# Kernel tuning notes

Measured on AMD Instinct MI355X. Metric: run time of the kernel, lower is better.

## Reference

```python
import jax, jax.numpy as jnp
import numpy as np

B, N, FIN, H, D = 2, 512, 128, 4, 64
NEG_SLOPE = 0.2


def setup_inputs() -> dict:
    key = jax.random.key(0)
    ks = jax.random.split(key, 5)
    x = jax.random.normal(ks[0], (B, N, FIN), dtype=jnp.float32)
    # xavier-ish scaled params
    W_proj = jax.random.normal(ks[1], (H, FIN, D), dtype=jnp.float32) * (1.0 / np.sqrt(FIN + D))
    b_proj = jnp.zeros((H, D), dtype=jnp.float32)
    W_cat_weight = jax.random.normal(ks[2], (H, D, 2 * D), dtype=jnp.float32) * (1.0 / np.sqrt(3 * D))
    W_cat_bias = jnp.zeros((H, D), dtype=jnp.float32)
    a = jax.random.normal(ks[3], (H, D), dtype=jnp.float32) * (1.0 / np.sqrt(D))
    bias_param = jnp.zeros((H * D,), dtype=jnp.float32)
    return {"x": x, "W_proj": W_proj, "b_proj": b_proj,
            "W_cat_weight": W_cat_weight, "W_cat_bias": W_cat_bias,
            "a": a, "bias_param": bias_param}


def reference(x, W_proj, b_proj, W_cat_weight, W_cat_bias, a, bias_param):
    # h[b,h,n,d] = W^h x_n + b^h
    h = jnp.einsum('bni,hid->bhnd', x, W_proj) + b_proj[None, :, None, :]
    d = h.shape[-1]
    # W_cat [h_i || h_j] == W1 h_i + W2 h_j  (avoids O(N^2*2D) concat tensor)
    W1 = W_cat_weight[:, :, :d]   # (H, D, D) acts on source node i
    W2 = W_cat_weight[:, :, d:]   # (H, D, D) acts on target node j
    zi = jnp.einsum('bhnd,hed->bhne', h, W1)  # (B,H,N,D)
    zj = jnp.einsum('bhnd,hed->bhne', h, W2)  # (B,H,N,D)
    # z[b,h,i,j,e] = zi[b,h,i,e] + zj[b,h,j,e] + bias, then LeakyReLU
    z = zi[:, :, :, None, :] + zj[:, :, None, :, :] + W_cat_bias[None, :, None, None, :]
    z = jnp.where(z >= 0, z, NEG_SLOPE * z)
    # e[b,h,i,j] = a_h . z
    e = jnp.einsum('bhije,he->bhij', z, a)
    attn = jax.nn.softmax(e, axis=-1)          # softmax over neighbors j
    out = jnp.einsum('bhij,bhjd->bhid', attn, h)  # (B,H,N,D)
    b_, h_, n_, d_ = out.shape
    out = out.transpose(0, 2, 1, 3).reshape(b_, n_, h_ * d_)  # concat heads
    out = out + bias_param
    return out
```

## Files before the change

kernel.cpp:

```cpp
#include <hip/hip_runtime.h>
#include <hip/hip_bf16.h>

#define NN 512
#define FIN 128
#define HH 4
#define DD 64
#define SW 68


__global__ __launch_bounds__(256) void proj_kernel(
    const float* __restrict__ x, const float* __restrict__ Wp,
    const float* __restrict__ bp, const float* __restrict__ Wc,
    const float* __restrict__ Wcb, const float* __restrict__ a,
    float* __restrict__ h_ws, float* __restrict__ azi_ws, float* __restrict__ azj_ws,
    float* __restrict__ adi_ws, float* __restrict__ adj_ws)
{
    int blk = blockIdx.x;
    int bh = blk >> 6;
    int n0 = (blk & 63) << 3;
    int b = bh >> 2, hh = bh & 3;

    __shared__ float xs[8 * FIN];
    __shared__ float hs[8][DD];
    __shared__ float Wcs[DD][2 * DD + 1];

    int t = threadIdx.x;

    ((float4*)xs)[t] = ((const float4*)(x + ((size_t)b * NN + n0) * FIN))[t];
    {
        const float4* wg = (const float4*)(Wc + (size_t)hh * DD * 2 * DD);
        #pragma unroll
        for (int k = 0; k < 8; ++k) {
            int idx = t + 256 * k;
            int r = idx >> 5, c4 = (idx & 31) * 4;
            float4 v = wg[idx];
            Wcs[r][c4] = v.x; Wcs[r][c4 + 1] = v.y;
            Wcs[r][c4 + 2] = v.z; Wcs[r][c4 + 3] = v.w;
        }
    }
    __syncthreads();

    int e = t & 63, w = t >> 6;
    const float* Wph = Wp + (size_t)hh * FIN * DD;
    float bpv = bp[hh * DD + e];
    float acc0 = bpv, acc1 = bpv;
    #pragma unroll 8
    for (int i = 0; i < FIN; ++i) {
        float wv = Wph[i * DD + e];
        acc0 = fmaf(xs[w * FIN + i], wv, acc0);
        acc1 = fmaf(xs[(w + 4) * FIN + i], wv, acc1);
    }
    hs[w][e] = acc0; hs[w + 4][e] = acc1;
    float* hg = h_ws + ((size_t)bh * NN + n0) * DD;
    hg[w * DD + e] = acc0; hg[(w + 4) * DD + e] = acc1;
    __syncthreads();

    float zb = Wcb[hh * DD + e];
    float zi0 = zb, zi1 = zb, zj0 = 0.f, zj1 = 0.f;
    #pragma unroll 8
    for (int d2 = 0; d2 < DD; ++d2) {
        float w1 = Wcs[e][d2];
        float w2 = Wcs[e][DD + d2];
        float h0 = hs[w][d2], h1 = hs[w + 4][d2];
        zi0 = fmaf(h0, w1, zi0); zi1 = fmaf(h1, w1, zi1);
        zj0 = fmaf(h0, w2, zj0); zj1 = fmaf(h1, w2, zj1);
    }

    float av = a[hh * DD + e];
    float p0 = av * zi0, p1 = av * zi1, q0 = av * zj0, q1 = av * zj1;
    #pragma unroll
    for (int off = 32; off; off >>= 1) {
        p0 += __shfl_xor(p0, off); p1 += __shfl_xor(p1, off);
        q0 += __shfl_xor(q0, off); q1 += __shfl_xor(q1, off);
    }
    if (e == 0) {
        adi_ws[bh * NN + n0 + w]     = 0.6f * p0;
        adi_ws[bh * NN + n0 + w + 4] = 0.6f * p1;
        adj_ws[bh * NN + n0 + w]     = 0.6f * q0;
        adj_ws[bh * NN + n0 + w + 4] = 0.6f * q1;
    }

    unsigned long long mask = __ballot(av >= 0.f);
    int np = __popcll(mask);
    int GP = (np + 3) >> 2;
    int below = __popcll(mask & ((1ull << e) - 1ull));
    int slot = (av >= 0.f) ? below : (4 * GP + (e - below));
    float pav = __builtin_fabsf(av);

    float* azib = azi_ws + ((size_t)bh * NN + n0) * SW;
    float* azjb = azj_ws + ((size_t)bh * NN + n0) * SW;
    azib[w * SW + slot]       = pav * zi0;
    azib[(w + 4) * SW + slot] = pav * zi1;
    azjb[w * SW + slot]       = pav * zj0;
    azjb[(w + 4) * SW + slot] = pav * zj1;
    int p1c = 4 * GP - np;
    if (e < 4) {
        int psl = (e < p1c) ? (np + e) : (4 * GP + 64 - np + (e - p1c));
        azib[w * SW + psl] = 0.f; azib[(w + 4) * SW + psl] = 0.f;
        azjb[w * SW + psl] = 0.f; azjb[(w + 4) * SW + psl] = 0.f;
    }
}

#define AZJ 0
#define HT  2176
#define ADJ 4224
__global__ __launch_bounds__(256) void attn6(
    const float* __restrict__ h_ws, const float* __restrict__ azi_ws,
    const float* __restrict__ azj_ws, const float* __restrict__ adi_ws,
    const float* __restrict__ adj_ws, const float* __restrict__ a,
    float* __restrict__ pacc, float* __restrict__ pm, float* __restrict__ ps)
{
    int blk = blockIdx.x;
    int js = blk & 15, is_ = (blk >> 4) & 7, bh = blk >> 7;
    int i0 = is_ << 6, j0 = js << 5, hh = bh & 3;
    int t = threadIdx.x, lane = t & 63, w = t >> 6;

    __shared__ float smA[64 * 68];
    __shared__ float eP[32 * 68];

    {
        const float4* src = (const float4*)(azi_ws + ((size_t)bh * NN + i0) * SW);
        float4* dst = (float4*)smA;
        #pragma unroll
        for (int k = 0; k < 5; ++k) {
            int idx = t + 256 * k;
            if (idx < 1088) dst[idx] = src[idx];
        }
    }
    __syncthreads();
    float4 azi4[17];
    #pragma unroll
    for (int k = 0; k < 17; ++k)
        azi4[k] = *(const float4*)&smA[lane * SW + 4 * k];
    float adiv = adi_ws[bh * NN + i0 + lane];
    __syncthreads();

    {
        const float4* sj = (const float4*)(azj_ws + ((size_t)bh * NN + j0) * SW);
        #pragma unroll
        for (int k = 0; k < 3; ++k) {
            int idx = t + 256 * k;
            if (idx < 544) ((float4*)&smA[AZJ])[idx] = sj[idx];
        }
        const float4* sh = (const float4*)(h_ws + ((size_t)bh * NN + j0) * DD);
        ((float4*)&smA[HT])[t]       = sh[t];
        ((float4*)&smA[HT])[t + 256] = sh[t + 256];
        if (t < 32) smA[ADJ + t] = adj_ws[bh * NN + j0 + t];
    }

    float av_e = a[hh * DD + lane];
    unsigned long long mask = __ballot(av_e >= 0.f);
    int GP = (__popcll(mask) + 3) >> 2;

    __syncthreads();

    #pragma unroll
    for (int jj = 0; jj < 8; ++jj) {
        int j = 8 * w + jj;
        const float4* aj = (const float4*)&smA[AZJ + j * SW];
        float adjv = smA[ADJ + j];
        float c0 = 0.f, c1 = 0.f, c2 = 0.f, c3 = 0.f;
        #pragma unroll
        for (int k = 0; k < 17; ++k) {
            float4 A = aj[k];
            float sg = (k < GP) ? 0.4f : -0.4f;
            c0 = fmaf(sg, __builtin_fabsf(azi4[k].x + A.x), c0);
            c1 = fmaf(sg, __builtin_fabsf(azi4[k].y + A.y), c1);
            c2 = fmaf(sg, __builtin_fabsf(azi4[k].z + A.z), c2);
            c3 = fmaf(sg, __builtin_fabsf(azi4[k].w + A.w), c3);
        }
        eP[j * SW + lane] = adiv + adjv + ((c0 + c1) + (c2 + c3));
    }
    __syncthreads();

    {
        int il = lane & 15, jq = lane >> 4;
        int iL = 16 * w + il;
        float e8[8];
        float m = -1e30f;
        #pragma unroll
        for (int jj = 0; jj < 8; ++jj) {
            e8[jj] = eP[(jq * 8 + jj) * SW + iL];
            m = fmaxf(m, e8[jj]);
        }
        m = fmaxf(m, __shfl_xor(m, 16));
        m = fmaxf(m, __shfl_xor(m, 32));
        float s = 0.f;
        #pragma unroll
        for (int jj = 0; jj < 8; ++jj) {
            float p = __expf(e8[jj] - m);
            s += p;
            eP[(jq * 8 + jj) * SW + iL] = p;
        }
        s += __shfl_xor(s, 16);
        s += __shfl_xor(s, 32);
        if (jq == 0) {
            pm[js * 4096 + bh * NN + i0 + iL] = m;
            ps[js * 4096 + bh * NN + i0 + iL] = s;
        }
    }
    __syncthreads();

    float acc[16];
    #pragma unroll
    for (int ii = 0; ii < 16; ++ii) acc[ii] = 0.f;
    #pragma unroll 8
    for (int j = 0; j < 32; ++j) {
        float hv = smA[HT + j * 64 + lane];
        const float4* pp = (const float4*)&eP[j * SW + 16 * w];
        float4 p0 = pp[0], p1 = pp[1], p2 = pp[2], p3 = pp[3];
        acc[0]  = fmaf(p0.x, hv, acc[0]);  acc[1]  = fmaf(p0.y, hv, acc[1]);
        acc[2]  = fmaf(p0.z, hv, acc[2]);  acc[3]  = fmaf(p0.w, hv, acc[3]);
        acc[4]  = fmaf(p1.x, hv, acc[4]);  acc[5]  = fmaf(p1.y, hv, acc[5]);
        acc[6]  = fmaf(p1.z, hv, acc[6]);  acc[7]  = fmaf(p1.w, hv, acc[7]);
        acc[8]  = fmaf(p2.x, hv, acc[8]);  acc[9]  = fmaf(p2.y, hv, acc[9]);
        acc[10] = fmaf(p2.z, hv, acc[10]); acc[11] = fmaf(p2.w, hv, acc[11]);
        acc[12] = fmaf(p3.x, hv, acc[12]); acc[13] = fmaf(p3.y, hv, acc[13]);
        acc[14] = fmaf(p3.z, hv, acc[14]); acc[15] = fmaf(p3.w, hv, acc[15]);
    }

    float* pb = pacc + ((size_t)(js * 8 + bh) * NN + i0 + 16 * w) * DD + lane;
    #pragma unroll
    for (int ii = 0; ii < 16; ++ii)
        pb[(size_t)ii * DD] = acc[ii];
}

__global__ __launch_bounds__(256) void combine_kernel(
    const float* __restrict__ pacc, const float* __restrict__ pm,
    const float* __restrict__ ps, const float* __restrict__ bias_param,
    float* __restrict__ out)
{
    int tid = blockIdx.x * 256 + threadIdx.x;
    int d = tid & 63;
    int row = tid >> 6;
    int bh = row >> 9, n = row & 511;
    int b = bh >> 2, hh = bh & 3;
    float mv[16];
    float m = -1e30f;
    #pragma unroll
    for (int p = 0; p < 16; ++p) { mv[p] = pm[p * 4096 + row]; m = fmaxf(m, mv[p]); }
    float denom = 0.f, acc = 0.f;
    #pragma unroll
    for (int p = 0; p < 16; ++p) {
        float wgt = __expf(mv[p] - m);
        denom = fmaf(ps[p * 4096 + row], wgt, denom);
        acc = fmaf(pacc[(size_t)p * 262144 + (size_t)row * 64 + d], wgt, acc);
    }
    out[((size_t)b * NN + n) * (HH * DD) + hh * DD + d] =
        acc / denom + bias_param[hh * DD + d];
}

extern "C" void kernel_launch(void* const* d_in, const int* in_sizes, int n_in,
                              void* d_out, int out_size, void* d_ws, size_t ws_size,
                              hipStream_t stream) {
    const float* x    = (const float*)d_in[0];
    const float* Wp   = (const float*)d_in[1];
    const float* bp   = (const float*)d_in[2];
    const float* Wc   = (const float*)d_in[3];
    const float* Wcb  = (const float*)d_in[4];
    const float* a    = (const float*)d_in[5];
    const float* bpar = (const float*)d_in[6];
    float* out = (float*)d_out;

    float* ws     = (float*)d_ws;
    float* h_ws   = ws;
    float* azi_ws = ws + 262144;
    float* azj_ws = ws + 540672;
    float* adi_ws = ws + 819200;
    float* adj_ws = ws + 823296;
    float* pacc   = ws + 827392;
    float* pm     = ws + 5021696;
    float* ps     = ws + 5087232;

    proj_kernel<<<dim3(512), dim3(256), 0, stream>>>(
        x, Wp, bp, Wc, Wcb, a, h_ws, azi_ws, azj_ws, adi_ws, adj_ws);
    attn6<<<dim3(1024), dim3(256), 0, stream>>>(
        h_ws, azi_ws, azj_ws, adi_ws, adj_ws, a, pacc, pm, ps);
    combine_kernel<<<dim3(1024), dim3(256), 0, stream>>>(
        pacc, pm, ps, bpar, out);
}
```

Before: 43.98 us.

## Broadcast zj and probabilities via readlane instead of LDS-staged sign-sorted layout

The projection kernel now writes plain zi/zj rows instead of the sign-sorted, |a|-scaled padded layout. The attention kernel loads zi directly into registers and broadcasts zj, the attention weights and the probability values across lanes with readlane, so the zj/h LDS staging and the pre-pass barriers go away. The cost is that the inner loop now needs a scalar readlane and a per-lane weight for every element, which adds SALU/VALU work compared with the previous sign-grouped constant multiplier. The h values are now read straight from global memory inside the PV loop.

Result: slower. 54.06 us (+22.9%).

```diff
diff --git a/kernel.cpp b/kernel.cpp
--- a/kernel.cpp
+++ b/kernel.cpp
@@ -5,14 +5,17 @@
 #define FIN 128
 #define HH 4
 #define DD 64
-#define SW 68
-
+
+
+__device__ __forceinline__ float rdlane(float v, int idx) {
+    return __int_as_float(__builtin_amdgcn_readlane(__float_as_int(v), idx));
+}
 
 __global__ __launch_bounds__(256) void proj_kernel(
     const float* __restrict__ x, const float* __restrict__ Wp,
     const float* __restrict__ bp, const float* __restrict__ Wc,
     const float* __restrict__ Wcb, const float* __restrict__ a,
-    float* __restrict__ h_ws, float* __restrict__ azi_ws, float* __restrict__ azj_ws,
+    float* __restrict__ h_ws, float* __restrict__ zi_ws, float* __restrict__ zj_ws,
     float* __restrict__ adi_ws, float* __restrict__ adj_ws)
 {
     int blk = blockIdx.x;
@@ -66,6 +69,11 @@
         zj0 = fmaf(h0, w2, zj0); zj1 = fmaf(h1, w2, zj1);
     }
 
+    float* zib = zi_ws + ((size_t)bh * NN + n0) * DD;
+    float* zjb = zj_ws + ((size_t)bh * NN + n0) * DD;
+    zib[w * DD + e] = zi0; zib[(w + 4) * DD + e] = zi1;
+    zjb[w * DD + e] = zj0; zjb[(w + 4) * DD + e] = zj1;
+
     float av = a[hh * DD + e];
     float p0 = av * zi0, p1 = av * zi1, q0 = av * zj0, q1 = av * zj1;
     #pragma unroll
@@ -79,34 +87,11 @@
         adj_ws[bh * NN + n0 + w]     = 0.6f * q0;
         adj_ws[bh * NN + n0 + w + 4] = 0.6f * q1;
     }
-
-    unsigned long long mask = __ballot(av >= 0.f);
-    int np = __popcll(mask);
-    int GP = (np + 3) >> 2;
-    int below = __popcll(mask & ((1ull << e) - 1ull));
-    int slot = (av >= 0.f) ? below : (4 * GP + (e - below));
-    float pav = __builtin_fabsf(av);
-
-    float* azib = azi_ws + ((size_t)bh * NN + n0) * SW;
-    float* azjb = azj_ws + ((size_t)bh * NN + n0) * SW;
-    azib[w * SW + slot]       = pav * zi0;
-    azib[(w + 4) * SW + slot] = pav * zi1;
-    azjb[w * SW + slot]       = pav * zj0;
-    azjb[(w + 4) * SW + slot] = pav * zj1;
-    int p1c = 4 * GP - np;
-    if (e < 4) {
-        int psl = (e < p1c) ? (np + e) : (4 * GP + 64 - np + (e - p1c));
-        azib[w * SW + psl] = 0.f; azib[(w + 4) * SW + psl] = 0.f;
-        azjb[w * SW + psl] = 0.f; azjb[(w + 4) * SW + psl] = 0.f;
-    }
-}
-
-#define AZJ 0
-#define HT  2176
-#define ADJ 4224
-__global__ __launch_bounds__(256) void attn6(
-    const float* __restrict__ h_ws, const float* __restrict__ azi_ws,
-    const float* __restrict__ azj_ws, const float* __restrict__ adi_ws,
+}
+
+__global__ __launch_bounds__(256) void attn7(
+    const float* __restrict__ h_ws, const float* __restrict__ zi_ws,
+    const float* __restrict__ zj_ws, const float* __restrict__ adi_ws,
     const float* __restrict__ adj_ws, const float* __restrict__ a,
     float* __restrict__ pacc, float* __restrict__ pm, float* __restrict__ ps)
 {
@@ -115,61 +100,37 @@
     int i0 = is_ << 6, j0 = js << 5, hh = bh & 3;
     int t = threadIdx.x, lane = t & 63, w = t >> 6;
 
-    __shared__ float smA[64 * 68];
-    __shared__ float eP[32 * 68];
-
+    __shared__ float eP[32 * 65];
+
+    float4 zi4[16];
     {
-        const float4* src = (const float4*)(azi_ws + ((size_t)bh * NN + i0) * SW);
-        float4* dst = (float4*)smA;
-        #pragma unroll
-        for (int k = 0; k < 5; ++k) {
-            int idx = t + 256 * k;
-            if (idx < 1088) dst[idx] = src[idx];
-        }
-    }
-    __syncthreads();
-    float4 azi4[17];
-    #pragma unroll
-    for (int k = 0; k < 17; ++k)
-        azi4[k] = *(const float4*)&smA[lane * SW + 4 * k];
-    float adiv = adi_ws[bh * NN + i0 + lane];
-    __syncthreads();
-
-    {
-        const float4* sj = (const float4*)(azj_ws + ((size_t)bh * NN + j0) * SW);
-        #pragma unroll
-        for (int k = 0; k < 3; ++k) {
-            int idx = t + 256 * k;
-            if (idx < 544) ((float4*)&smA[AZJ])[idx] = sj[idx];
-        }
-        const float4* sh = (const float4*)(h_ws + ((size_t)bh * NN + j0) * DD);
-        ((float4*)&smA[HT])[t]       = sh[t];
-        ((float4*)&smA[HT])[t + 256] = sh[t + 256];
-        if (t < 32) smA[ADJ + t] = adj_ws[bh * NN + j0 + t];
-    }
-
-    float av_e = a[hh * DD + lane];
-    unsigned long long mask = __ballot(av_e >= 0.f);
-    int GP = (__popcll(mask) + 3) >> 2;
-
-    __syncthreads();
+        const float4* zr = (const float4*)(zi_ws + ((size_t)bh * NN + i0 + lane) * DD);
+        #pragma unroll
+        for (int k = 0; k < 16; ++k) zi4[k] = zr[k];
+    }
+    float vu   = 0.4f * a[hh * DD + lane];
+    float vadj = adj_ws[bh * NN + j0 + (lane & 31)];
+    float vadi = adi_ws[bh * NN + i0 + lane];
 
     #pragma unroll
     for (int jj = 0; jj < 8; ++jj) {
         int j = 8 * w + jj;
-        const float4* aj = (const float4*)&smA[AZJ + j * SW];
-        float adjv = smA[ADJ + j];
-        float c0 = 0.f, c1 = 0.f, c2 = 0.f, c3 = 0.f;
-        #pragma unroll
-        for (int k = 0; k < 17; ++k) {
-            float4 A = aj[k];
-            float sg = (k < GP) ? 0.4f : -0.4f;
-            c0 = fmaf(sg, __builtin_fabsf(azi4[k].x + A.x), c0);
-            c1 = fmaf(sg, __builtin_fabsf(azi4[k].y + A.y), c1);
-            c2 = fmaf(sg, __builtin_fabsf(azi4[k].z + A.z), c2);
-            c3 = fmaf(sg, __builtin_fabsf(azi4[k].w + A.w), c3);
-        }
-        eP[j * SW + lane] = adiv + adjv + ((c0 + c1) + (c2 + c3));
+        float vzj = zj_ws[((size_t)bh * NN + j0 + j) * DD + lane];
+        float sadj = rdlane(vadj, j);
+        float a0 = 0.f, a1 = 0.f, a2 = 0.f, a3 = 0.f;
+        #pragma unroll
+        for (int k = 0; k < 16; ++k) {
+            float4 z = zi4[k];
+            float s0 = rdlane(vzj, 4 * k + 0), u0 = rdlane(vu, 4 * k + 0);
+            float s1 = rdlane(vzj, 4 * k + 1), u1 = rdlane(vu, 4 * k + 1);
+            float s2 = rdlane(vzj, 4 * k + 2), u2 = rdlane(vu, 4 * k + 2);
+            float s3 = rdlane(vzj, 4 * k + 3), u3 = rdlane(vu, 4 * k + 3);
+            a0 = fmaf(u0, __builtin_fabsf(z.x + s0), a0);
+            a1 = fmaf(u1, __builtin_fabsf(z.y + s1), a1);
+            a2 = fmaf(u2, __builtin_fabsf(z.z + s2), a2);
+            a3 = fmaf(u3, __builtin_fabsf(z.w + s3), a3);
+        }
+        eP[j * 65 + lane] = vadi + sadj + ((a0 + a1) + (a2 + a3));
     }
     __syncthreads();
 
@@ -180,7 +141,7 @@
         float m = -1e30f;
         #pragma unroll
         for (int jj = 0; jj < 8; ++jj) {
-            e8[jj] = eP[(jq * 8 + jj) * SW + iL];
+            e8[jj] = eP[(jq * 8 + jj) * 65 + iL];
             m = fmaxf(m, e8[jj]);
         }
         m = fmaxf(m, __shfl_xor(m, 16));
@@ -190,7 +151,7 @@
         for (int jj = 0; jj < 8; ++jj) {
             float p = __expf(e8[jj] - m);
             s += p;
-            eP[(jq * 8 + jj) * SW + iL] = p;
+            eP[(jq * 8 + jj) * 65 + iL] = p;
         }
         s += __shfl_xor(s, 16);
         s += __shfl_xor(s, 32);
@@ -206,17 +167,13 @@
     for (int ii = 0; ii < 16; ++ii) acc[ii] = 0.f;
     #pragma unroll 8
     for (int j = 0; j < 32; ++j) {
-        float hv = smA[HT + j * 64 + lane];
-        const float4* pp = (const float4*)&eP[j * SW + 16 * w];
-        float4 p0 = pp[0], p1 = pp[1], p2 = pp[2], p3 = pp[3];
-        acc[0]  = fmaf(p0.x, hv, acc[0]);  acc[1]  = fmaf(p0.y, hv, acc[1]);
-        acc[2]  = fmaf(p0.z, hv, acc[2]);  acc[3]  = fmaf(p0.w, hv, acc[3]);
-        acc[4]  = fmaf(p1.x, hv, acc[4]);  acc[5]  = fmaf(p1.y, hv, acc[5]);
-        acc[6]  = fmaf(p1.z, hv, acc[6]);  acc[7]  = fmaf(p1.w, hv, acc[7]);
-        acc[8]  = fmaf(p2.x, hv, acc[8]);  acc[9]  = fmaf(p2.y, hv, acc[9]);
-        acc[10] = fmaf(p2.z, hv, acc[10]); acc[11] = fmaf(p2.w, hv, acc[11]);
-        acc[12] = fmaf(p3.x, hv, acc[12]); acc[13] = fmaf(p3.y, hv, acc[13]);
-        acc[14] = fmaf(p3.z, hv, acc[14]); acc[15] = fmaf(p3.w, hv, acc[15]);
+        float vh = h_ws[((size_t)bh * NN + j0 + j) * DD + lane];
+        float vp = eP[j * 65 + lane];
+        #pragma unroll
+        for (int ii = 0; ii < 16; ++ii) {
+            float sp = rdlane(vp, 16 * w + ii);
+            acc[ii] = fmaf(sp, vh, acc[ii]);
+        }
     }
 
     float* pb = pacc + ((size_t)(js * 8 + bh) * NN + i0 + 16 * w) * DD + lane;
@@ -264,18 +221,18 @@
 
     float* ws     = (float*)d_ws;
     float* h_ws   = ws;
-    float* azi_ws = ws + 262144;
-    float* azj_ws = ws + 540672;
-    float* adi_ws = ws + 819200;
-    float* adj_ws = ws + 823296;
-    float* pacc   = ws + 827392;
-    float* pm     = ws + 5021696;
-    float* ps     = ws + 5087232;
+    float* zi_ws  = ws + 262144;
+    float* zj_ws  = ws + 524288;
+    float* adi_ws = ws + 786432;
+    float* adj_ws = ws + 790528;
+    float* pacc   = ws + 794624;
+    float* pm     = ws + 4988928;
+    float* ps     = ws + 5054464;
 
     proj_kernel<<<dim3(512), dim3(256), 0, stream>>>(
-        x, Wp, bp, Wc, Wcb, a, h_ws, azi_ws, azj_ws, adi_ws, adj_ws);
-    attn6<<<dim3(1024), dim3(256), 0, stream>>>(
-        h_ws, azi_ws, azj_ws, adi_ws, adj_ws, a, pacc, pm, ps);
+        x, Wp, bp, Wc, Wcb, a, h_ws, zi_ws, zj_ws, adi_ws, adj_ws);
+    attn7<<<dim3(1024), dim3(256), 0, stream>>>(
+        h_ws, zi_ws, zj_ws, adi_ws, adj_ws, a, pacc, pm, ps);
     combine_kernel<<<dim3(1024), dim3(256), 0, stream>>>(
         pacc, pm, ps, bpar, out);
 }
```

## Double attention i-tile to 128 rows and broadcast probabilities via readlane

Applied to the files above, without the earlier changes.

The attention kernel now processes 128 query rows per block instead of 64, so each lane holds two rows of zi in registers and reuses every loaded zj element for both. The launch is halved to 512 blocks and the shared-memory layout is merged into one padded buffer. In the P·V stage, probabilities are broadcast across the wavefront with readlane instead of float4 LDS reads, with 32 accumulators per thread. This trades higher register pressure (34 float4 for zi plus 32 accumulators) and fewer blocks for less LDS traffic and better reuse, so occupancy may drop.

Result: slower. 48.75 us (+10.8%).

```diff
diff --git a/kernel.cpp b/kernel.cpp
--- a/kernel.cpp
+++ b/kernel.cpp
@@ -7,6 +7,10 @@
 #define DD 64
 #define SW 68
 
+
+__device__ __forceinline__ float rdlane(float v, int idx) {
+    return __int_as_float(__builtin_amdgcn_readlane(__float_as_int(v), idx));
+}
 
 __global__ __launch_bounds__(256) void proj_kernel(
     const float* __restrict__ x, const float* __restrict__ Wp,
@@ -101,38 +105,44 @@
     }
 }
 
-#define AZJ 0
-#define HT  2176
-#define ADJ 4224
-__global__ __launch_bounds__(256) void attn6(
+#define ZJS 0
+#define HS  2176
+#define ADJS 4224
+#define EPo 4256
+__global__ __launch_bounds__(256, 2) void attn9(
     const float* __restrict__ h_ws, const float* __restrict__ azi_ws,
     const float* __restrict__ azj_ws, const float* __restrict__ adi_ws,
     const float* __restrict__ adj_ws, const float* __restrict__ a,
     float* __restrict__ pacc, float* __restrict__ pm, float* __restrict__ ps)
 {
     int blk = blockIdx.x;
-    int js = blk & 15, is_ = (blk >> 4) & 7, bh = blk >> 7;
-    int i0 = is_ << 6, j0 = js << 5, hh = bh & 3;
-    int t = threadIdx.x, lane = t & 63, w = t >> 6;
-
-    __shared__ float smA[64 * 68];
-    __shared__ float eP[32 * 68];
+    int js = blk & 15, is_ = (blk >> 4) & 3, bh = blk >> 6;
+    int i0 = is_ << 7, j0 = js << 5, hh = bh & 3;
+    int t = threadIdx.x, lane = t & 63;
+    int w = __builtin_amdgcn_readfirstlane(t >> 6);
+
+    __shared__ float smem[128 * 72];
 
     {
         const float4* src = (const float4*)(azi_ws + ((size_t)bh * NN + i0) * SW);
-        float4* dst = (float4*)smA;
-        #pragma unroll
-        for (int k = 0; k < 5; ++k) {
+        #pragma unroll
+        for (int k = 0; k < 9; ++k) {
             int idx = t + 256 * k;
-            if (idx < 1088) dst[idx] = src[idx];
-        }
-    }
-    __syncthreads();
-    float4 azi4[17];
-    #pragma unroll
-    for (int k = 0; k < 17; ++k)
-        azi4[k] = *(const float4*)&smA[lane * SW + 4 * k];
-    float adiv = adi_ws[bh * NN + i0 + lane];
+            if (idx < 2176) {
+                int r = idx / 17, c = idx % 17;
+                *(float4*)&smem[r * 72 + c * 4] = src[idx];
+            }
+        }
+    }
+    __syncthreads();
+    float4 ziA[17], ziB[17];
+    #pragma unroll
+    for (int k = 0; k < 17; ++k) {
+        ziA[k] = *(const float4*)&smem[lane * 72 + 4 * k];
+        ziB[k] = *(const float4*)&smem[(lane + 64) * 72 + 4 * k];
+    }
+    float adi0 = adi_ws[bh * NN + i0 + lane];
+    float adi1 = adi_ws[bh * NN + i0 + 64 + lane];
     __syncthreads();
 
     {
@@ -140,12 +150,12 @@
         #pragma unroll
         for (int k = 0; k < 3; ++k) {
             int idx = t + 256 * k;
-            if (idx < 544) ((float4*)&smA[AZJ])[idx] = sj[idx];
+            if (idx < 544) ((float4*)&smem[ZJS])[idx] = sj[idx];
         }
         const float4* sh = (const float4*)(h_ws + ((size_t)bh * NN + j0) * DD);
-        ((float4*)&smA[HT])[t]       = sh[t];
-        ((float4*)&smA[HT])[t + 256] = sh[t + 256];
-        if (t < 32) smA[ADJ + t] = adj_ws[bh * NN + j0 + t];
+        ((float4*)&smem[HS])[t] = sh[t];
+        ((float4*)&smem[HS])[t + 256] = sh[t + 256];
+        if (t < 32) smem[ADJS + t] = adj_ws[bh * NN + j0 + t];
     }
 
     float av_e = a[hh * DD + lane];
@@ -157,72 +167,73 @@
     #pragma unroll
     for (int jj = 0; jj < 8; ++jj) {
         int j = 8 * w + jj;
-        const float4* aj = (const float4*)&smA[AZJ + j * SW];
-        float adjv = smA[ADJ + j];
-        float c0 = 0.f, c1 = 0.f, c2 = 0.f, c3 = 0.f;
+        const float4* zjr = (const float4*)&smem[ZJS + j * SW];
+        float adjv = smem[ADJS + j];
+        float a0 = 0.f, a1 = 0.f, b0 = 0.f, b1 = 0.f;
         #pragma unroll
         for (int k = 0; k < 17; ++k) {
-            float4 A = aj[k];
+            float4 z = zjr[k];
             float sg = (k < GP) ? 0.4f : -0.4f;
-            c0 = fmaf(sg, __builtin_fabsf(azi4[k].x + A.x), c0);
-            c1 = fmaf(sg, __builtin_fabsf(azi4[k].y + A.y), c1);
-            c2 = fmaf(sg, __builtin_fabsf(azi4[k].z + A.z), c2);
-            c3 = fmaf(sg, __builtin_fabsf(azi4[k].w + A.w), c3);
-        }
-        eP[j * SW + lane] = adiv + adjv + ((c0 + c1) + (c2 + c3));
-    }
-    __syncthreads();
-
-    {
-        int il = lane & 15, jq = lane >> 4;
-        int iL = 16 * w + il;
-        float e8[8];
+            a0 = fmaf(sg, __builtin_fabsf(ziA[k].x + z.x), a0);
+            a1 = fmaf(sg, __builtin_fabsf(ziA[k].y + z.y), a1);
+            a0 = fmaf(sg, __builtin_fabsf(ziA[k].z + z.z), a0);
+            a1 = fmaf(sg, __builtin_fabsf(ziA[k].w + z.w), a1);
+            b0 = fmaf(sg, __builtin_fabsf(ziB[k].x + z.x), b0);
+            b1 = fmaf(sg, __builtin_fabsf(ziB[k].y + z.y), b1);
+            b0 = fmaf(sg, __builtin_fabsf(ziB[k].z + z.z), b0);
+            b1 = fmaf(sg, __builtin_fabsf(ziB[k].w + z.w), b1);
+        }
+        smem[EPo + j * 132 + lane]      = adi0 + adjv + (a0 + a1);
+        smem[EPo + j * 132 + 64 + lane] = adi1 + adjv + (b0 + b1);
+    }
+    __syncthreads();
+
+    {
+        int r = t >> 1, jh = t & 1;
+        float e16[16];
         float m = -1e30f;
         #pragma unroll
-        for (int jj = 0; jj < 8; ++jj) {
-            e8[jj] = eP[(jq * 8 + jj) * SW + iL];
-            m = fmaxf(m, e8[jj]);
-        }
-        m = fmaxf(m, __shfl_xor(m, 16));
-        m = fmaxf(m, __shfl_xor(m, 32));
+        for (int jj = 0; jj < 16; ++jj) {
+            e16[jj] = smem[EPo + (16 * jh + jj) * 132 + r];
+            m = fmaxf(m, e16[jj]);
+        }
+        m = fmaxf(m, __shfl_xor(m, 1));
         float s = 0.f;
         #pragma unroll
-        for (int jj = 0; jj < 8; ++jj) {
-            float p = __expf(e8[jj] - m);
+        for (int jj = 0; jj < 16; ++jj) {
+            float p = __expf(e16[jj] - m);
             s += p;
-            eP[(jq * 8 + jj) * SW + iL] = p;
-        }
-        s += __shfl_xor(s, 16);
-        s += __shfl_xor(s, 32);
-        if (jq == 0) {
-            pm[js * 4096 + bh * NN + i0 + iL] = m;
-            ps[js * 4096 + bh * NN + i0 + iL] = s;
-        }
-    }
-    __syncthreads();
-
-    float acc[16];
-    #pragma unroll
-    for (int ii = 0; ii < 16; ++ii) acc[ii] = 0.f;
-    #pragma unroll 8
-    for (int j = 0; j < 32; ++j) {
-        float hv = smA[HT + j * 64 + lane];
-        const float4* pp = (const float4*)&eP[j * SW + 16 * w];
-        float4 p0 = pp[0], p1 = pp[1], p2 = pp[2], p3 = pp[3];
-        acc[0]  = fmaf(p0.x, hv, acc[0]);  acc[1]  = fmaf(p0.y, hv, acc[1]);
-        acc[2]  = fmaf(p0.z, hv, acc[2]);  acc[3]  = fmaf(p0.w, hv, acc[3]);
-        acc[4]  = fmaf(p1.x, hv, acc[4]);  acc[5]  = fmaf(p1.y, hv, acc[5]);
-        acc[6]  = fmaf(p1.z, hv, acc[6]);  acc[7]  = fmaf(p1.w, hv, acc[7]);
-        acc[8]  = fmaf(p2.x, hv, acc[8]);  acc[9]  = fmaf(p2.y, hv, acc[9]);
-        acc[10] = fmaf(p2.z, hv, acc[10]); acc[11] = fmaf(p2.w, hv, acc[11]);
-        acc[12] = fmaf(p3.x, hv, acc[12]); acc[13] = fmaf(p3.y, hv, acc[13]);
-        acc[14] = fmaf(p3.z, hv, acc[14]); acc[15] = fmaf(p3.w, hv, acc[15]);
-    }
-
-    float* pb = pacc + ((size_t)(js * 8 + bh) * NN + i0 + 16 * w) * DD + lane;
-    #pragma unroll
-    for (int ii = 0; ii < 16; ++ii)
-        pb[(size_t)ii * DD] = acc[ii];
+            smem[EPo + (16 * jh + jj) * 132 + r] = p;
+        }
+        s += __shfl_xor(s, 1);
+        if (jh == 0) {
+            pm[js * 4096 + bh * NN + i0 + r] = m;
+            ps[js * 4096 + bh * NN + i0 + r] = s;
+        }
+    }
+    __syncthreads();
+
+    {
+        int hi = (w >> 1) * 64;
+        int base = (w & 1) * 32;
+        float acc[32];
+        #pragma unroll
+        for (int q = 0; q < 32; ++q) acc[q] = 0.f;
+        #pragma unroll 4
+        for (int j = 0; j < 32; ++j) {
+            float vh = smem[HS + j * 64 + lane];
+            float vp = smem[EPo + j * 132 + hi + lane];
+            #pragma unroll
+            for (int ii = 0; ii < 32; ++ii) {
+                float sp = rdlane(vp, base + ii);
+                acc[ii] = fmaf(sp, vh, acc[ii]);
+            }
+        }
+        float* pb = pacc + ((size_t)(js * 8 + bh) * NN + i0 + 32 * w) * DD + lane;
+        #pragma unroll
+        for (int q = 0; q < 32; ++q)
+            pb[(size_t)q * DD] = acc[q];
+    }
 }
 
 __global__ __launch_bounds__(256) void combine_kernel(
@@ -274,7 +285,7 @@
 
     proj_kernel<<<dim3(512), dim3(256), 0, stream>>>(
         x, Wp, bp, Wc, Wcb, a, h_ws, azi_ws, azj_ws, adi_ws, adj_ws);
-    attn6<<<dim3(1024), dim3(256), 0, stream>>>(
+    attn9<<<dim3(512), dim3(256), 0, stream>>>(
         h_ws, azi_ws, azj_ws, adi_ws, adj_ws, a, pacc, pm, ps);
     combine_kernel<<<dim3(1024), dim3(256), 0, stream>>>(
         pacc, pm, ps, bpar, out);
```

## Store azi/azj in chunk-major float4 layout and load azi directly to registers

Applied to the files above, without the earlier changes.

The projection kernel now writes the scaled zi/zj vectors in a [bh][chunk of 4][node] float4 layout instead of padded rows of 68 floats. The attention kernel then loads each thread's 17 azi float4s straight from global memory with coalesced accesses, dropping the shared-memory staging pass and two barriers. Shared memory is merged into one buffer. The azj tile is read from LDS column-wise by chunk, which changes the bank access pattern. Scattered 4-byte writes in the projection kernel become more strided.

Result: slower. 45.55 us (+3.6%).

```diff
diff --git a/kernel.cpp b/kernel.cpp
--- a/kernel.cpp
+++ b/kernel.cpp
@@ -12,7 +12,7 @@
     const float* __restrict__ x, const float* __restrict__ Wp,
     const float* __restrict__ bp, const float* __restrict__ Wc,
     const float* __restrict__ Wcb, const float* __restrict__ a,
-    float* __restrict__ h_ws, float* __restrict__ azi_ws, float* __restrict__ azj_ws,
+    float* __restrict__ h_ws, float* __restrict__ azi_c, float* __restrict__ azj_c,
     float* __restrict__ adi_ws, float* __restrict__ adj_ws)
 {
     int blk = blockIdx.x;
@@ -87,26 +87,29 @@
     int slot = (av >= 0.f) ? below : (4 * GP + (e - below));
     float pav = __builtin_fabsf(av);
 
-    float* azib = azi_ws + ((size_t)bh * NN + n0) * SW;
-    float* azjb = azj_ws + ((size_t)bh * NN + n0) * SW;
-    azib[w * SW + slot]       = pav * zi0;
-    azib[(w + 4) * SW + slot] = pav * zi1;
-    azjb[w * SW + slot]       = pav * zj0;
-    azjb[(w + 4) * SW + slot] = pav * zj1;
+    {
+        size_t a0 = ((size_t)(bh * 17 + (slot >> 2)) * NN + n0 + w) * 4 + (slot & 3);
+        size_t a1 = ((size_t)(bh * 17 + (slot >> 2)) * NN + n0 + w + 4) * 4 + (slot & 3);
+        azi_c[a0] = pav * zi0; azi_c[a1] = pav * zi1;
+        azj_c[a0] = pav * zj0; azj_c[a1] = pav * zj1;
+    }
     int p1c = 4 * GP - np;
     if (e < 4) {
         int psl = (e < p1c) ? (np + e) : (4 * GP + 64 - np + (e - p1c));
-        azib[w * SW + psl] = 0.f; azib[(w + 4) * SW + psl] = 0.f;
-        azjb[w * SW + psl] = 0.f; azjb[(w + 4) * SW + psl] = 0.f;
-    }
-}
-
-#define AZJ 0
-#define HT  2176
-#define ADJ 4224
-__global__ __launch_bounds__(256) void attn6(
-    const float* __restrict__ h_ws, const float* __restrict__ azi_ws,
-    const float* __restrict__ azj_ws, const float* __restrict__ adi_ws,
+        size_t a0 = ((size_t)(bh * 17 + (psl >> 2)) * NN + n0 + w) * 4 + (psl & 3);
+        size_t a1 = ((size_t)(bh * 17 + (psl >> 2)) * NN + n0 + w + 4) * 4 + (psl & 3);
+        azi_c[a0] = 0.f; azi_c[a1] = 0.f;
+        azj_c[a0] = 0.f; azj_c[a1] = 0.f;
+    }
+}
+
+#define ZJC  0
+#define HSo  2176
+#define ADJo 4224
+#define EPo  4256
+__global__ __launch_bounds__(256) void attn6v3(
+    const float* __restrict__ h_ws, const float* __restrict__ azi_c,
+    const float* __restrict__ azj_c, const float* __restrict__ adi_ws,
     const float* __restrict__ adj_ws, const float* __restrict__ a,
     float* __restrict__ pacc, float* __restrict__ pm, float* __restrict__ ps)
 {
@@ -115,38 +118,29 @@
     int i0 = is_ << 6, j0 = js << 5, hh = bh & 3;
     int t = threadIdx.x, lane = t & 63, w = t >> 6;
 
-    __shared__ float smA[64 * 68];
-    __shared__ float eP[32 * 68];
-
-    {
-        const float4* src = (const float4*)(azi_ws + ((size_t)bh * NN + i0) * SW);
-        float4* dst = (float4*)smA;
-        #pragma unroll
-        for (int k = 0; k < 5; ++k) {
-            int idx = t + 256 * k;
-            if (idx < 1088) dst[idx] = src[idx];
-        }
-    }
-    __syncthreads();
-    float4 azi4[17];
-    #pragma unroll
-    for (int k = 0; k < 17; ++k)
-        azi4[k] = *(const float4*)&smA[lane * SW + 4 * k];
-    float adiv = adi_ws[bh * NN + i0 + lane];
-    __syncthreads();
-
-    {
-        const float4* sj = (const float4*)(azj_ws + ((size_t)bh * NN + j0) * SW);
+    __shared__ float smem[6432];
+
+    {
+        float4* dstJ = (float4*)(smem + ZJC);
         #pragma unroll
         for (int k = 0; k < 3; ++k) {
             int idx = t + 256 * k;
-            if (idx < 544) ((float4*)&smA[AZJ])[idx] = sj[idx];
+            if (idx < 544) {
+                int c = idx >> 5, r = idx & 31;
+                dstJ[idx] = ((const float4*)azj_c)[(size_t)(bh * 17 + c) * NN + j0 + r];
+            }
         }
         const float4* sh = (const float4*)(h_ws + ((size_t)bh * NN + j0) * DD);
-        ((float4*)&smA[HT])[t]       = sh[t];
-        ((float4*)&smA[HT])[t + 256] = sh[t + 256];
-        if (t < 32) smA[ADJ + t] = adj_ws[bh * NN + j0 + t];
-    }
+        ((float4*)(smem + HSo))[t]       = sh[t];
+        ((float4*)(smem + HSo))[t + 256] = sh[t + 256];
+        if (t < 32) smem[ADJo + t] = adj_ws[bh * NN + j0 + t];
+    }
+
+    float4 azi4[17];
+    #pragma unroll
+    for (int k = 0; k < 17; ++k)
+        azi4[k] = ((const float4*)azi_c)[(size_t)(bh * 17 + k) * NN + i0 + lane];
+    float adiv = adi_ws[bh * NN + i0 + lane];
 
     float av_e = a[hh * DD + lane];
     unsigned long long mask = __ballot(av_e >= 0.f);
@@ -157,19 +151,19 @@
     #pragma unroll
     for (int jj = 0; jj < 8; ++jj) {
         int j = 8 * w + jj;
-        const float4* aj = (const float4*)&smA[AZJ + j * SW];
-        float adjv = smA[ADJ + j];
+        float adjv = smem[ADJo + j];
         float c0 = 0.f, c1 = 0.f, c2 = 0.f, c3 = 0.f;
+        const float4* ZJ = (const float4*)(smem + ZJC);
         #pragma unroll
         for (int k = 0; k < 17; ++k) {
-            float4 A = aj[k];
+            float4 A = ZJ[k * 32 + j];
             float sg = (k < GP) ? 0.4f : -0.4f;
             c0 = fmaf(sg, __builtin_fabsf(azi4[k].x + A.x), c0);
             c1 = fmaf(sg, __builtin_fabsf(azi4[k].y + A.y), c1);
             c2 = fmaf(sg, __builtin_fabsf(azi4[k].z + A.z), c2);
             c3 = fmaf(sg, __builtin_fabsf(azi4[k].w + A.w), c3);
         }
-        eP[j * SW + lane] = adiv + adjv + ((c0 + c1) + (c2 + c3));
+        smem[EPo + j * SW + lane] = adiv + adjv + ((c0 + c1) + (c2 + c3));
     }
     __syncthreads();
 
@@ -180,7 +174,7 @@
         float m = -1e30f;
         #pragma unroll
         for (int jj = 0; jj < 8; ++jj) {
-            e8[jj] = eP[(jq * 8 + jj) * SW + iL];
+            e8[jj] = smem[EPo + (jq * 8 + jj) * SW + iL];
             m = fmaxf(m, e8[jj]);
         }
         m = fmaxf(m, __shfl_xor(m, 16));
@@ -190,7 +184,7 @@
         for (int jj = 0; jj < 8; ++jj) {
             float p = __expf(e8[jj] - m);
             s += p;
-            eP[(jq * 8 + jj) * SW + iL] = p;
+            smem[EPo + (jq * 8 + jj) * SW + iL] = p;
         }
         s += __shfl_xor(s, 16);
         s += __shfl_xor(s, 32);
@@ -206,8 +200,8 @@
     for (int ii = 0; ii < 16; ++ii) acc[ii] = 0.f;
     #pragma unroll 8
     for (int j = 0; j < 32; ++j) {
-        float hv = smA[HT + j * 64 + lane];
-        const float4* pp = (const float4*)&eP[j * SW + 16 * w];
+        float hv = smem[HSo + j * 64 + lane];
+        const float4* pp = (const float4*)(smem + EPo + j * SW + 16 * w);
         float4 p0 = pp[0], p1 = pp[1], p2 = pp[2], p3 = pp[3];
         acc[0]  = fmaf(p0.x, hv, acc[0]);  acc[1]  = fmaf(p0.y, hv, acc[1]);
         acc[2]  = fmaf(p0.z, hv, acc[2]);  acc[3]  = fmaf(p0.w, hv, acc[3]);
@@ -264,8 +258,8 @@
 
     float* ws     = (float*)d_ws;
     float* h_ws   = ws;
-    float* azi_ws = ws + 262144;
-    float* azj_ws = ws + 540672;
+    float* azi_c  = ws + 262144;
+    float* azj_c  = ws + 540672;
     float* adi_ws = ws + 819200;
     float* adj_ws = ws + 823296;
     float* pacc   = ws + 827392;
@@ -273,9 +267,9 @@
     float* ps     = ws + 5087232;
 
     proj_kernel<<<dim3(512), dim3(256), 0, stream>>>(
-        x, Wp, bp, Wc, Wcb, a, h_ws, azi_ws, azj_ws, adi_ws, adj_ws);
-    attn6<<<dim3(1024), dim3(256), 0, stream>>>(
-        h_ws, azi_ws, azj_ws, adi_ws, adj_ws, a, pacc, pm, ps);
+        x, Wp, bp, Wc, Wcb, a, h_ws, azi_c, azj_c, adi_ws, adj_ws);
+    attn6v3<<<dim3(1024), dim3(256), 0, stream>>>(
+        h_ws, azi_c, azj_c, adi_ws, adj_ws, a, pacc, pm, ps);
     combine_kernel<<<dim3(1024), dim3(256), 0, stream>>>(
         pacc, pm, ps, bpar, out);
 }
```
